# Kernel tuning notes

Hardware: AMD Instinct MI355X
Metric: run time of the kernel (lower is better)

## Reference

```python
import jax, jax.numpy as jnp
import numpy as np

N_NODES = 50000
N_EDGES = 640000
D = 128


def _sage_conv(x, src, dst, W_l, b, W_r, n_nodes):
    # PyG SAGEConv with mean aggregation:
    #   out = lin_l(mean_{j in N(i)} x_j) + lin_r(x_i)
    msg = x[src]                                              # [E, D] gather
    agg = jax.ops.segment_sum(msg, dst, num_segments=n_nodes)  # [N, D] scatter-add
    cnt = jax.ops.segment_sum(jnp.ones((src.shape[0], 1), x.dtype), dst,
                              num_segments=n_nodes)            # [N, 1]
    agg = agg / jnp.maximum(cnt, 1.0)                          # mean (0 if no neighbors)
    return agg @ W_l + b + x @ W_r


def setup_inputs() -> dict:
    key = jax.random.key(0)
    ks = jax.random.split(key, 8)
    s = 1.0 / np.sqrt(D)
    x = jax.random.normal(ks[0], (N_NODES, D), dtype=jnp.float32)
    edge_index = jax.random.randint(ks[1], (2, N_EDGES), 0, N_NODES, dtype=jnp.int64)
    return {
        "x": x,
        "edge_index": edge_index,
        "W_l1": jax.random.normal(ks[2], (D, D), dtype=jnp.float32) * s,
        "b1": jnp.zeros((D,), jnp.float32),
        "W_r1": jax.random.normal(ks[3], (D, D), dtype=jnp.float32) * s,
        "W_l2": jax.random.normal(ks[4], (D, D), dtype=jnp.float32) * s,
        "b2": jnp.zeros((D,), jnp.float32),
        "W_r2": jax.random.normal(ks[5], (D, D), dtype=jnp.float32) * s,
        "W_l3": jax.random.normal(ks[6], (D, D), dtype=jnp.float32) * s,
        "b3": jnp.zeros((D,), jnp.float32),
        "W_r3": jax.random.normal(ks[7], (D, D), dtype=jnp.float32) * s,
    }


def reference(x, edge_index, W_l1, b1, W_r1, W_l2, b2, W_r2, W_l3, b3, W_r3):
    src, dst = edge_index[0], edge_index[1]
    n = x.shape[0]
    h = jax.nn.relu(_sage_conv(x, src, dst, W_l1, b1, W_r1, n))
    h = jax.nn.relu(_sage_conv(h, src, dst, W_l2, b2, W_r2, n))
    h = _sage_conv(h, src, dst, W_l3, b3, W_r3, n)
    return h
```

## Files before the change

### kernel.cpp

```cpp
#include <hip/hip_runtime.h>
#include <stdint.h>


using bf16x8 = __attribute__((ext_vector_type(8))) __bf16;
using f32x16 = __attribute__((ext_vector_type(16))) float;

__device__ inline unsigned short f2bf(float v) {
    uint32_t u = __float_as_uint(v);
    uint32_t r = u + 0x7FFF + ((u >> 16) & 1);
    return (unsigned short)(r >> 16);
}
__device__ inline float bf2f(unsigned short h) {
    return __uint_as_float(((uint32_t)h) << 16);
}
__device__ inline float uf(uint32_t u) { return __uint_as_float(u); }

__device__ inline void split8(const float* v, bf16x8& h, bf16x8& l) {
    #pragma unroll
    for (int j = 0; j < 8; ++j) {
        unsigned short hs = f2bf(v[j]);
        unsigned short ls = f2bf(v[j] - bf2f(hs));
        ((unsigned short*)&h)[j] = hs;
        ((unsigned short*)&l)[j] = ls;
    }
}

__global__ void k_hist(const int* __restrict__ dst, int* __restrict__ deg, int E)
{
    int i = blockIdx.x * blockDim.x + threadIdx.x;
    int stride = gridDim.x * blockDim.x;
    for (; i < E; i += stride) atomicAdd(&deg[dst[i]], 1);
}

__global__ __launch_bounds__(1024) void k_scan(const int* __restrict__ deg,
                                               int* __restrict__ rp,
                                               int* __restrict__ cur, int n)
{
    __shared__ int wsum[16];
    __shared__ int carry_s;
    int tid = threadIdx.x, lane = tid & 63, w = tid >> 6;
    if (tid == 0) carry_s = 0;
    __syncthreads();
    for (int base = 0; base < n; base += 4096) {
        int i = base + tid * 4;
        int4 v = make_int4(0, 0, 0, 0);
        if (i + 3 < n) v = *(const int4*)(deg + i);
        else {
            if (i     < n) v.x = deg[i];
            if (i + 1 < n) v.y = deg[i + 1];
            if (i + 2 < n) v.z = deg[i + 2];
            if (i + 3 < n) v.w = deg[i + 3];
        }
        int t = v.x + v.y + v.z + v.w;
        int s = t;
        #pragma unroll
        for (int d = 1; d < 64; d <<= 1) { int u = __shfl_up(s, d); if (lane >= d) s += u; }
        if (lane == 63) wsum[w] = s;
        __syncthreads();
        if (w == 0 && lane < 16) {
            int u = wsum[lane];
            #pragma unroll
            for (int d = 1; d < 16; d <<= 1) { int y = __shfl_up(u, d); if (lane >= d) u += y; }
            wsum[lane] = u;
        }
        __syncthreads();
        int carry = carry_s;
        int off = carry + (w ? wsum[w - 1] : 0) + (s - t);
        int r0 = off, r1 = r0 + v.x, r2 = r1 + v.y, r3 = r2 + v.z;
        if (i + 3 < n) {
            *(int4*)(rp + i)  = make_int4(r0, r1, r2, r3);
            *(int4*)(cur + i) = make_int4(r0, r1, r2, r3);
        } else {
            if (i     < n) { rp[i]     = r0; cur[i]     = r0; }
            if (i + 1 < n) { rp[i + 1] = r1; cur[i + 1] = r1; }
            if (i + 2 < n) { rp[i + 2] = r2; cur[i + 2] = r2; }
            if (i + 3 < n) { rp[i + 3] = r3; cur[i + 3] = r3; }
        }
        __syncthreads();
        if (tid == 1023) carry_s = carry + wsum[15];
    }
    __syncthreads();
    if (tid == 0) rp[n] = carry_s;
}

__global__ void k_fill(const int* __restrict__ src, const int* __restrict__ dst,
                       int* __restrict__ cur, int* __restrict__ col, int E)
{
    int i = blockIdx.x * blockDim.x + threadIdx.x;
    int stride = gridDim.x * blockDim.x;
    for (; i < E; i += stride) {
        int p = atomicAdd(&cur[dst[i]], 1);
        col[p] = src[i];
    }
}

__global__ __launch_bounds__(256) void k_splitW(const float* __restrict__ Wl,
                                                const float* __restrict__ Wr,
                                                unsigned short* __restrict__ img)
{
    int idx = blockIdx.x * 256 + threadIdx.x;
    int ch  = idx >> 13;
    int rem = idx & 8191;
    int c   = rem >> 6;
    int kk  = rem & 63;
    float v = (ch < 2 ? Wl : Wr)[((ch & 1) * 64 + kk) * 128 + c];
    unsigned short h = f2bf(v);
    unsigned short l = f2bf(v - bf2f(h));
    img[ch * 16384 + rem]        = h;
    img[ch * 16384 + 8192 + rem] = l;
}

template<int INF32, int OUTF32>
__global__ __launch_bounds__(256) void k_fused(const float* __restrict__ xf,
                                               const unsigned short* __restrict__ inH,
                                               const unsigned short* __restrict__ inL,
                                               const int* __restrict__ rp,
                                               const int* __restrict__ col,
                                               const unsigned short* __restrict__ wimg,
                                               const float* __restrict__ bias,
                                               float* __restrict__ outF,
                                               unsigned short* __restrict__ oH,
                                               unsigned short* __restrict__ oL,
                                               int relu, int nNodes)
{
    __shared__ float aggF[64 * 132];
    const int tid  = threadIdx.x;
    const int wave = tid >> 6, l = tid & 63;
    const int lh   = l >> 5, l31 = l & 31;
    const int wm = wave >> 1, wn = wave & 1;
    const int m0w = wm * 32, n0w = wn * 64;
    const int node0 = blockIdx.x * 64;

    #pragma unroll 1
    for (int j = 0; j < 16; ++j) {
        const int nl = wave * 16 + j;
        const int n  = node0 + nl;
        int s = 0, e = 0;
        if (n < nNodes) { s = rp[n]; e = rp[n + 1]; }
        float a0 = 0.f, a1 = 0.f, b0 = 0.f, b1 = 0.f;
        float c0a = 0.f, c1a = 0.f, d0a = 0.f, d1a = 0.f;
        int i = s;
        if (INF32) {
            for (; i + 4 <= e; i += 4) {
                int e0 = col[i], e1 = col[i+1], e2 = col[i+2], e3 = col[i+3];
                float2 v0 = *(const float2*)(xf + (size_t)e0 * 128 + 2 * l);
                float2 v1 = *(const float2*)(xf + (size_t)e1 * 128 + 2 * l);
                float2 v2 = *(const float2*)(xf + (size_t)e2 * 128 + 2 * l);
                float2 v3 = *(const float2*)(xf + (size_t)e3 * 128 + 2 * l);
                a0 += v0.x; a1 += v0.y; b0 += v1.x; b1 += v1.y;
                c0a += v2.x; c1a += v2.y; d0a += v3.x; d1a += v3.y;
            }
            for (; i < e; ++i) {
                float2 v0 = *(const float2*)(xf + (size_t)col[i] * 128 + 2 * l);
                a0 += v0.x; a1 += v0.y;
            }
        } else {
            for (; i + 4 <= e; i += 4) {
                int e0 = col[i], e1 = col[i+1], e2 = col[i+2], e3 = col[i+3];
                uint32_t h0 = *(const uint32_t*)(inH + (size_t)e0 * 128 + 2 * l);
                uint32_t g0 = *(const uint32_t*)(inL + (size_t)e0 * 128 + 2 * l);
                uint32_t h1 = *(const uint32_t*)(inH + (size_t)e1 * 128 + 2 * l);
                uint32_t g1 = *(const uint32_t*)(inL + (size_t)e1 * 128 + 2 * l);
                uint32_t h2 = *(const uint32_t*)(inH + (size_t)e2 * 128 + 2 * l);
                uint32_t g2 = *(const uint32_t*)(inL + (size_t)e2 * 128 + 2 * l);
                uint32_t h3 = *(const uint32_t*)(inH + (size_t)e3 * 128 + 2 * l);
                uint32_t g3 = *(const uint32_t*)(inL + (size_t)e3 * 128 + 2 * l);
                a0 += uf(h0 << 16) + uf(g0 << 16);
                a1 += uf(h0 & 0xffff0000u) + uf(g0 & 0xffff0000u);
                b0 += uf(h1 << 16) + uf(g1 << 16);
                b1 += uf(h1 & 0xffff0000u) + uf(g1 & 0xffff0000u);
                c0a += uf(h2 << 16) + uf(g2 << 16);
                c1a += uf(h2 & 0xffff0000u) + uf(g2 & 0xffff0000u);
                d0a += uf(h3 << 16) + uf(g3 << 16);
                d1a += uf(h3 & 0xffff0000u) + uf(g3 & 0xffff0000u);
            }
            for (; i < e; ++i) {
                int e0 = col[i];
                uint32_t h0 = *(const uint32_t*)(inH + (size_t)e0 * 128 + 2 * l);
                uint32_t g0 = *(const uint32_t*)(inL + (size_t)e0 * 128 + 2 * l);
                a0 += uf(h0 << 16) + uf(g0 << 16);
                a1 += uf(h0 & 0xffff0000u) + uf(g0 & 0xffff0000u);
            }
        }
        float inv = (e > s) ? (1.f / (float)(e - s)) : 0.f;
        float2 o;
        o.x = ((a0 + b0) + (c0a + d0a)) * inv;
        o.y = ((a1 + b1) + (c1a + d1a)) * inv;
        *(float2*)&aggF[nl * 132 + 2 * l] = o;
    }
    __syncthreads();

    f32x16 acc0, acc1;
    #pragma unroll
    for (int i = 0; i < 16; ++i) { acc0[i] = 0.f; acc1[i] = 0.f; }

    const int rowA_loc  = m0w + l31;
    const int rowA_glob = min(node0 + rowA_loc, nNodes - 1);
    const int c0 = n0w + l31, c1 = c0 + 32;

    #pragma unroll
    for (int ch = 0; ch < 4; ++ch) {
        const unsigned short* wb = wimg + ch * 16384;
        #pragma unroll
        for (int ks = 0; ks < 4; ++ks) {
            const int sg   = ks * 2 + lh;
            const int koff = (ch & 1) * 64 + sg * 8;
            bf16x8 a_h, a_l;
            if (ch < 2) {
                float v[8];
                const float* p = &aggF[rowA_loc * 132 + koff];
                *(float4*)v       = *(const float4*)p;
                *(float4*)(v + 4) = *(const float4*)(p + 4);
                split8(v, a_h, a_l);
            } else if (INF32) {
                float v[8];
                const float* p = xf + (size_t)rowA_glob * 128 + koff;
                *(float4*)v       = *(const float4*)p;
                *(float4*)(v + 4) = *(const float4*)(p + 4);
                split8(v, a_h, a_l);
            } else {
                a_h = *(const bf16x8*)(inH + (size_t)rowA_glob * 128 + koff);
                a_l = *(const bf16x8*)(inL + (size_t)rowA_glob * 128 + koff);
            }
            bf16x8 b_h0 = *(const bf16x8*)(wb + c0 * 64 + sg * 8);
            bf16x8 b_l0 = *(const bf16x8*)(wb + 8192 + c0 * 64 + sg * 8);
            bf16x8 b_h1 = *(const bf16x8*)(wb + c1 * 64 + sg * 8);
            bf16x8 b_l1 = *(const bf16x8*)(wb + 8192 + c1 * 64 + sg * 8);
            acc0 = __builtin_amdgcn_mfma_f32_32x32x16_bf16(a_h, b_h0, acc0, 0, 0, 0);
            acc1 = __builtin_amdgcn_mfma_f32_32x32x16_bf16(a_h, b_h1, acc1, 0, 0, 0);
            acc0 = __builtin_amdgcn_mfma_f32_32x32x16_bf16(a_h, b_l0, acc0, 0, 0, 0);
            acc1 = __builtin_amdgcn_mfma_f32_32x32x16_bf16(a_h, b_l1, acc1, 0, 0, 0);
            acc0 = __builtin_amdgcn_mfma_f32_32x32x16_bf16(a_l, b_h0, acc0, 0, 0, 0);
            acc1 = __builtin_amdgcn_mfma_f32_32x32x16_bf16(a_l, b_h1, acc1, 0, 0, 0);
        }
    }

    __syncthreads();
    const float bv0 = bias[n0w + l31];
    const float bv1 = bias[n0w + 32 + l31];
    #pragma unroll
    for (int reg = 0; reg < 16; ++reg) {
        int row = (reg & 3) + 8 * (reg >> 2) + 4 * lh;
        int rl  = m0w + row;
        float v0 = acc0[reg] + bv0;
        float v1 = acc1[reg] + bv1;
        if (relu) { v0 = fmaxf(v0, 0.f); v1 = fmaxf(v1, 0.f); }
        aggF[rl * 132 + n0w + l31]      = v0;
        aggF[rl * 132 + n0w + 32 + l31] = v1;
    }
    __syncthreads();
    {
        const int rl = tid >> 2;
        const int gn = node0 + rl;
        if (gn < nNodes) {
            const int cq = (tid & 3) * 32;
            const float* p = &aggF[rl * 132 + cq];
            if (OUTF32) {
                float* o = outF + (size_t)gn * 128 + cq;
                #pragma unroll
                for (int q = 0; q < 8; ++q)
                    *(float4*)(o + q * 4) = *(const float4*)(p + q * 4);
            } else {
                #pragma unroll
                for (int g = 0; g < 4; ++g) {
                    float v[8];
                    *(float4*)v       = *(const float4*)(p + g * 8);
                    *(float4*)(v + 4) = *(const float4*)(p + g * 8 + 4);
                    unsigned short hs[8], ls[8];
                    #pragma unroll
                    for (int q = 0; q < 8; ++q) {
                        hs[q] = f2bf(v[q]);
                        ls[q] = f2bf(v[q] - bf2f(hs[q]));
                    }
                    *(uint4*)(oH + (size_t)gn * 128 + cq + g * 8) = *(uint4*)hs;
                    *(uint4*)(oL + (size_t)gn * 128 + cq + g * 8) = *(uint4*)ls;
                }
            }
        }
    }
}

extern "C" void kernel_launch(void* const* d_in, const int* in_sizes, int n_in,
                              void* d_out, int out_size, void* d_ws, size_t ws_size,
                              hipStream_t stream)
{
    const float* x   = (const float*)d_in[0];
    const int*   ei  = (const int*)d_in[1];
    const float* Wl1 = (const float*)d_in[2];
    const float* b1  = (const float*)d_in[3];
    const float* Wr1 = (const float*)d_in[4];
    const float* Wl2 = (const float*)d_in[5];
    const float* b2  = (const float*)d_in[6];
    const float* Wr2 = (const float*)d_in[7];
    const float* Wl3 = (const float*)d_in[8];
    const float* b3  = (const float*)d_in[9];
    const float* Wr3 = (const float*)d_in[10];

    int N = in_sizes[0] / 128;
    int E = in_sizes[1] / 2;
    const int* srcp = ei;
    const int* dstp = ei + E;
    size_t P = (size_t)N * 128;

    unsigned short* Hh = (unsigned short*)d_ws;
    unsigned short* Hl = Hh + P;
    int* deg = (int*)(Hl + P);
    int* rp  = deg + ((N + 3) & ~3);
    int* cur = rp + ((N + 4) & ~3);
    int* col = cur + ((N + 3) & ~3);
    unsigned short* Wimg = (unsigned short*)(col + ((E + 3) & ~3));

    unsigned short* Oh = (unsigned short*)d_out;
    unsigned short* Ol = Oh + P;
    float* out = (float*)d_out;

    hipMemsetAsync(deg, 0, (size_t)N * sizeof(int), stream);
    k_hist<<<1024, 256, 0, stream>>>(dstp, deg, E);
    k_scan<<<1, 1024, 0, stream>>>(deg, rp, cur, N);
    k_fill<<<1024, 256, 0, stream>>>(srcp, dstp, cur, col, E);

    k_splitW<<<128, 256, 0, stream>>>(Wl1, Wr1, Wimg);
    k_splitW<<<128, 256, 0, stream>>>(Wl2, Wr2, Wimg + 65536);
    k_splitW<<<128, 256, 0, stream>>>(Wl3, Wr3, Wimg + 131072);

    int gb = (N + 63) / 64;
    k_fused<1, 0><<<gb, 256, 0, stream>>>(x, nullptr, nullptr, rp, col,
                                          Wimg, b1, nullptr, Oh, Ol, 1, N);
    k_fused<0, 0><<<gb, 256, 0, stream>>>(nullptr, Oh, Ol, rp, col,
                                          Wimg + 65536, b2, nullptr, Hh, Hl, 1, N);
    k_fused<0, 1><<<gb, 256, 0, stream>>>(nullptr, Hh, Hl, rp, col,
                                          Wimg + 131072, b3, out, nullptr, nullptr, 0, N);
}
```

Measured before the change: 487.9 us.

## Interleave bf16 hi/lo into packed words and use 512-thread blocks

Stores the split bf16 activations as one packed 32-bit word per element (hi in the upper half, lo in the lower) instead of two separate planes. Each gather now fetches one 8-byte load per lane rather than two 4-byte loads from different arrays, which halves the number of scattered memory transactions. Blocks grow to 512 threads (8 waves), so each wave aggregates 8 nodes and computes one 32-column MFMA tile. This adds parallelism per block but may reduce occupancy and cost extra unpacking ALU work in the GEMM A-operand load.

```diff
diff --git a/kernel.cpp b/kernel.cpp
--- a/kernel.cpp
+++ b/kernel.cpp
@@ -14,14 +14,18 @@
     return __uint_as_float(((uint32_t)h) << 16);
 }
 __device__ inline float uf(uint32_t u) { return __uint_as_float(u); }
+__device__ inline uint32_t packbf(float v) {
+    unsigned short hs = f2bf(v);
+    unsigned short ls = f2bf(v - bf2f(hs));
+    return ((uint32_t)hs << 16) | ls;
+}
 
 __device__ inline void split8(const float* v, bf16x8& h, bf16x8& l) {
     #pragma unroll
     for (int j = 0; j < 8; ++j) {
         unsigned short hs = f2bf(v[j]);
-        unsigned short ls = f2bf(v[j] - bf2f(hs));
         ((unsigned short*)&h)[j] = hs;
-        ((unsigned short*)&l)[j] = ls;
+        ((unsigned short*)&l)[j] = f2bf(v[j] - bf2f(hs));
     }
 }
 
@@ -105,35 +109,32 @@
     int kk  = rem & 63;
     float v = (ch < 2 ? Wl : Wr)[((ch & 1) * 64 + kk) * 128 + c];
     unsigned short h = f2bf(v);
-    unsigned short l = f2bf(v - bf2f(h));
     img[ch * 16384 + rem]        = h;
-    img[ch * 16384 + 8192 + rem] = l;
+    img[ch * 16384 + 8192 + rem] = f2bf(v - bf2f(h));
 }
 
 template<int INF32, int OUTF32>
-__global__ __launch_bounds__(256) void k_fused(const float* __restrict__ xf,
-                                               const unsigned short* __restrict__ inH,
-                                               const unsigned short* __restrict__ inL,
+__global__ __launch_bounds__(512) void k_fused(const float* __restrict__ xf,
+                                               const uint32_t* __restrict__ inP,
                                                const int* __restrict__ rp,
                                                const int* __restrict__ col,
                                                const unsigned short* __restrict__ wimg,
                                                const float* __restrict__ bias,
                                                float* __restrict__ outF,
-                                               unsigned short* __restrict__ oH,
-                                               unsigned short* __restrict__ oL,
+                                               uint32_t* __restrict__ outP,
                                                int relu, int nNodes)
 {
     __shared__ float aggF[64 * 132];
     const int tid  = threadIdx.x;
     const int wave = tid >> 6, l = tid & 63;
     const int lh   = l >> 5, l31 = l & 31;
-    const int wm = wave >> 1, wn = wave & 1;
-    const int m0w = wm * 32, n0w = wn * 64;
+    const int wm = wave >> 2, wn = wave & 3;
+    const int m0w = wm * 32;
     const int node0 = blockIdx.x * 64;
 
     #pragma unroll 1
-    for (int j = 0; j < 16; ++j) {
-        const int nl = wave * 16 + j;
+    for (int j = 0; j < 8; ++j) {
+        const int nl = wave * 8 + j;
         const int n  = node0 + nl;
         int s = 0, e = 0;
         if (n < nNodes) { s = rp[n]; e = rp[n + 1]; }
@@ -157,29 +158,23 @@
         } else {
             for (; i + 4 <= e; i += 4) {
                 int e0 = col[i], e1 = col[i+1], e2 = col[i+2], e3 = col[i+3];
-                uint32_t h0 = *(const uint32_t*)(inH + (size_t)e0 * 128 + 2 * l);
-                uint32_t g0 = *(const uint32_t*)(inL + (size_t)e0 * 128 + 2 * l);
-                uint32_t h1 = *(const uint32_t*)(inH + (size_t)e1 * 128 + 2 * l);
-                uint32_t g1 = *(const uint32_t*)(inL + (size_t)e1 * 128 + 2 * l);
-                uint32_t h2 = *(const uint32_t*)(inH + (size_t)e2 * 128 + 2 * l);
-                uint32_t g2 = *(const uint32_t*)(inL + (size_t)e2 * 128 + 2 * l);
-                uint32_t h3 = *(const uint32_t*)(inH + (size_t)e3 * 128 + 2 * l);
-                uint32_t g3 = *(const uint32_t*)(inL + (size_t)e3 * 128 + 2 * l);
-                a0 += uf(h0 << 16) + uf(g0 << 16);
-                a1 += uf(h0 & 0xffff0000u) + uf(g0 & 0xffff0000u);
-                b0 += uf(h1 << 16) + uf(g1 << 16);
-                b1 += uf(h1 & 0xffff0000u) + uf(g1 & 0xffff0000u);
-                c0a += uf(h2 << 16) + uf(g2 << 16);
-                c1a += uf(h2 & 0xffff0000u) + uf(g2 & 0xffff0000u);
-                d0a += uf(h3 << 16) + uf(g3 << 16);
-                d1a += uf(h3 & 0xffff0000u) + uf(g3 & 0xffff0000u);
+                uint2 u0 = *(const uint2*)(inP + (size_t)e0 * 128 + 2 * l);
+                uint2 u1 = *(const uint2*)(inP + (size_t)e1 * 128 + 2 * l);
+                uint2 u2 = *(const uint2*)(inP + (size_t)e2 * 128 + 2 * l);
+                uint2 u3 = *(const uint2*)(inP + (size_t)e3 * 128 + 2 * l);
+                a0 += uf(u0.x & 0xffff0000u) + uf(u0.x << 16);
+                a1 += uf(u0.y & 0xffff0000u) + uf(u0.y << 16);
+                b0 += uf(u1.x & 0xffff0000u) + uf(u1.x << 16);
+                b1 += uf(u1.y & 0xffff0000u) + uf(u1.y << 16);
+                c0a += uf(u2.x & 0xffff0000u) + uf(u2.x << 16);
+                c1a += uf(u2.y & 0xffff0000u) + uf(u2.y << 16);
+                d0a += uf(u3.x & 0xffff0000u) + uf(u3.x << 16);
+                d1a += uf(u3.y & 0xffff0000u) + uf(u3.y << 16);
             }
             for (; i < e; ++i) {
-                int e0 = col[i];
-                uint32_t h0 = *(const uint32_t*)(inH + (size_t)e0 * 128 + 2 * l);
-                uint32_t g0 = *(const uint32_t*)(inL + (size_t)e0 * 128 + 2 * l);
-                a0 += uf(h0 << 16) + uf(g0 << 16);
-                a1 += uf(h0 & 0xffff0000u) + uf(g0 & 0xffff0000u);
+                uint2 u0 = *(const uint2*)(inP + (size_t)col[i] * 128 + 2 * l);
+                a0 += uf(u0.x & 0xffff0000u) + uf(u0.x << 16);
+                a1 += uf(u0.y & 0xffff0000u) + uf(u0.y << 16);
             }
         }
         float inv = (e > s) ? (1.f / (float)(e - s)) : 0.f;
@@ -190,13 +185,13 @@
     }
     __syncthreads();
 
-    f32x16 acc0, acc1;
+    f32x16 acc;
     #pragma unroll
-    for (int i = 0; i < 16; ++i) { acc0[i] = 0.f; acc1[i] = 0.f; }
+    for (int i = 0; i < 16; ++i) acc[i] = 0.f;
 
     const int rowA_loc  = m0w + l31;
     const int rowA_glob = min(node0 + rowA_loc, nNodes - 1);
-    const int c0 = n0w + l31, c1 = c0 + 32;
+    const int c = wn * 32 + l31;
 
     #pragma unroll
     for (int ch = 0; ch < 4; ++ch) {
@@ -219,61 +214,55 @@
                 *(float4*)(v + 4) = *(const float4*)(p + 4);
                 split8(v, a_h, a_l);
             } else {
-                a_h = *(const bf16x8*)(inH + (size_t)rowA_glob * 128 + koff);
-                a_l = *(const bf16x8*)(inL + (size_t)rowA_glob * 128 + koff);
-            }
-            bf16x8 b_h0 = *(const bf16x8*)(wb + c0 * 64 + sg * 8);
-            bf16x8 b_l0 = *(const bf16x8*)(wb + 8192 + c0 * 64 + sg * 8);
-            bf16x8 b_h1 = *(const bf16x8*)(wb + c1 * 64 + sg * 8);
-            bf16x8 b_l1 = *(const bf16x8*)(wb + 8192 + c1 * 64 + sg * 8);
-            acc0 = __builtin_amdgcn_mfma_f32_32x32x16_bf16(a_h, b_h0, acc0, 0, 0, 0);
-            acc1 = __builtin_amdgcn_mfma_f32_32x32x16_bf16(a_h, b_h1, acc1, 0, 0, 0);
-            acc0 = __builtin_amdgcn_mfma_f32_32x32x16_bf16(a_h, b_l0, acc0, 0, 0, 0);
-            acc1 = __builtin_amdgcn_mfma_f32_32x32x16_bf16(a_h, b_l1, acc1, 0, 0, 0);
-            acc0 = __builtin_amdgcn_mfma_f32_32x32x16_bf16(a_l, b_h0, acc0, 0, 0, 0);
-            acc1 = __builtin_amdgcn_mfma_f32_32x32x16_bf16(a_l, b_h1, acc1, 0, 0, 0);
-        }
-    }
-
-    __syncthreads();
-    const float bv0 = bias[n0w + l31];
-    const float bv1 = bias[n0w + 32 + l31];
+                const uint32_t* p = inP + (size_t)rowA_glob * 128 + koff;
+                uint4 q0 = *(const uint4*)p;
+                uint4 q1 = *(const uint4*)(p + 4);
+                uint32_t q[8] = {q0.x, q0.y, q0.z, q0.w, q1.x, q1.y, q1.z, q1.w};
+                #pragma unroll
+                for (int jj = 0; jj < 8; ++jj) {
+                    ((unsigned short*)&a_h)[jj] = (unsigned short)(q[jj] >> 16);
+                    ((unsigned short*)&a_l)[jj] = (unsigned short)(q[jj] & 0xffffu);
+                }
+            }
+            bf16x8 b_h = *(const bf16x8*)(wb + c * 64 + sg * 8);
+            bf16x8 b_l = *(const bf16x8*)(wb + 8192 + c * 64 + sg * 8);
+            acc = __builtin_amdgcn_mfma_f32_32x32x16_bf16(a_h, b_h, acc, 0, 0, 0);
+            acc = __builtin_amdgcn_mfma_f32_32x32x16_bf16(a_h, b_l, acc, 0, 0, 0);
+            acc = __builtin_amdgcn_mfma_f32_32x32x16_bf16(a_l, b_h, acc, 0, 0, 0);
+        }
+    }
+
+    __syncthreads();
+    const float bv = bias[c];
     #pragma unroll
     for (int reg = 0; reg < 16; ++reg) {
         int row = (reg & 3) + 8 * (reg >> 2) + 4 * lh;
-        int rl  = m0w + row;
-        float v0 = acc0[reg] + bv0;
-        float v1 = acc1[reg] + bv1;
-        if (relu) { v0 = fmaxf(v0, 0.f); v1 = fmaxf(v1, 0.f); }
-        aggF[rl * 132 + n0w + l31]      = v0;
-        aggF[rl * 132 + n0w + 32 + l31] = v1;
+        float v = acc[reg] + bv;
+        if (relu) v = fmaxf(v, 0.f);
+        aggF[(m0w + row) * 132 + c] = v;
     }
     __syncthreads();
     {
-        const int rl = tid >> 2;
+        const int rl = tid >> 3;
         const int gn = node0 + rl;
         if (gn < nNodes) {
-            const int cq = (tid & 3) * 32;
+            const int cq = (tid & 7) * 16;
             const float* p = &aggF[rl * 132 + cq];
             if (OUTF32) {
                 float* o = outF + (size_t)gn * 128 + cq;
                 #pragma unroll
-                for (int q = 0; q < 8; ++q)
+                for (int q = 0; q < 4; ++q)
                     *(float4*)(o + q * 4) = *(const float4*)(p + q * 4);
             } else {
+                uint32_t* o = outP + (size_t)gn * 128 + cq;
                 #pragma unroll
                 for (int g = 0; g < 4; ++g) {
-                    float v[8];
-                    *(float4*)v       = *(const float4*)(p + g * 8);
-                    *(float4*)(v + 4) = *(const float4*)(p + g * 8 + 4);
-                    unsigned short hs[8], ls[8];
-                    #pragma unroll
-                    for (int q = 0; q < 8; ++q) {
-                        hs[q] = f2bf(v[q]);
-                        ls[q] = f2bf(v[q] - bf2f(hs[q]));
-                    }
-                    *(uint4*)(oH + (size_t)gn * 128 + cq + g * 8) = *(uint4*)hs;
-                    *(uint4*)(oL + (size_t)gn * 128 + cq + g * 8) = *(uint4*)ls;
+                    float v[4];
+                    *(float4*)v = *(const float4*)(p + g * 4);
+                    uint4 u;
+                    u.x = packbf(v[0]); u.y = packbf(v[1]);
+                    u.z = packbf(v[2]); u.w = packbf(v[3]);
+                    *(uint4*)(o + g * 4) = u;
                 }
             }
         }
@@ -302,16 +291,14 @@
     const int* dstp = ei + E;
     size_t P = (size_t)N * 128;
 
-    unsigned short* Hh = (unsigned short*)d_ws;
-    unsigned short* Hl = Hh + P;
-    int* deg = (int*)(Hl + P);
+    uint32_t* Hpk = (uint32_t*)d_ws;
+    int* deg = (int*)(Hpk + P);
     int* rp  = deg + ((N + 3) & ~3);
     int* cur = rp + ((N + 4) & ~3);
     int* col = cur + ((N + 3) & ~3);
     unsigned short* Wimg = (unsigned short*)(col + ((E + 3) & ~3));
 
-    unsigned short* Oh = (unsigned short*)d_out;
-    unsigned short* Ol = Oh + P;
+    uint32_t* Opk = (uint32_t*)d_out;
     float* out = (float*)d_out;
 
     hipMemsetAsync(deg, 0, (size_t)N * sizeof(int), stream);
@@ -324,10 +311,10 @@
     k_splitW<<<128, 256, 0, stream>>>(Wl3, Wr3, Wimg + 131072);
 
     int gb = (N + 63) / 64;
-    k_fused<1, 0><<<gb, 256, 0, stream>>>(x, nullptr, nullptr, rp, col,
-                                          Wimg, b1, nullptr, Oh, Ol, 1, N);
-    k_fused<0, 0><<<gb, 256, 0, stream>>>(nullptr, Oh, Ol, rp, col,
-                                          Wimg + 65536, b2, nullptr, Hh, Hl, 1, N);
-    k_fused<0, 1><<<gb, 256, 0, stream>>>(nullptr, Hh, Hl, rp, col,
-                                          Wimg + 131072, b3, out, nullptr, nullptr, 0, N);
-}
+    k_fused<1, 0><<<gb, 512, 0, stream>>>(x, nullptr, rp, col,
+                                          Wimg, b1, nullptr, Opk, 1, N);
+    k_fused<0, 0><<<gb, 512, 0, stream>>>(nullptr, Opk, rp, col,
+                                          Wimg + 65536, b2, nullptr, Hpk, 1, N);
+    k_fused<0, 1><<<gb, 512, 0, stream>>>(nullptr, Hpk, rp, col,
+                                          Wimg + 131072, b3, out, nullptr, 0, N);
+}
```

Result: slower. 525.3 us (+7.7%).
